# Performance work log

Measured on AMD Instinct MI355X. Metric: run time of the kernel, lower is better.

## Reference

```python
import jax, jax.numpy as jnp
import numpy as np

N_NODES = 50000
N_EDGES = 800000
NUM_HEADS = 4
HEAD_DIM = 32
IN_DIM = 128
NEG_SLOPE = 0.2


def setup_inputs() -> dict:
    key = jax.random.key(0)
    k1, k2, k3, k4, k5, k6 = jax.random.split(key, 6)
    x = jax.random.normal(k1, (N_NODES, IN_DIM), dtype=jnp.float32)
    W = jax.random.normal(k2, (NUM_HEADS * HEAD_DIM, IN_DIM), dtype=jnp.float32) * 0.05
    attn_l = jax.random.normal(k3, (NUM_HEADS, HEAD_DIM), dtype=jnp.float32) * 0.05
    attn_r = jax.random.normal(k4, (NUM_HEADS, HEAD_DIM), dtype=jnp.float32) * 0.05
    src = jax.random.randint(k5, (N_EDGES,), 0, N_NODES, dtype=jnp.int32)
    dst = jnp.sort(jax.random.randint(k6, (N_EDGES,), 0, N_NODES, dtype=jnp.int32))
    return {"x": x, "W": W, "attn_l": attn_l, "attn_r": attn_r, "src": src, "dst": dst}


def reference(x, W, attn_l, attn_r, src, dst):
    N = x.shape[0]
    H, D = attn_l.shape
    # linear projection: [N, H*D] -> [N, H, D]
    feat = (x @ W.T).reshape(N, H, D)
    # per-node attention terms  [N, H]
    el = jnp.einsum('nhd,hd->nh', feat, attn_l)
    er = jnp.einsum('nhd,hd->nh', feat, attn_r)
    # per-edge logits (u_add_v) + leaky relu  [E, H]
    e = el[src] + er[dst]
    e = jnp.where(e > 0, e, NEG_SLOPE * e)
    # edge softmax segmented by destination node
    e_max = jax.ops.segment_max(e, dst, num_segments=N)          # [N, H]
    e_exp = jnp.exp(e - e_max[dst])                              # [E, H]
    denom = jax.ops.segment_sum(e_exp, dst, num_segments=N)     # [N, H]
    alpha = e_exp / denom[dst]                                   # [E, H]
    # attention-weighted neighbor aggregation  [N, H, D]
    out = jax.ops.segment_sum(alpha[:, :, None] * feat[src], dst, num_segments=N)
    return out.reshape(N, H * D)
```

## Files before the change

### kernel.cpp

```cpp
#include <hip/hip_runtime.h>
#include <math.h>

#define NN 50000
#define NE 800000
#define NH 4
#define HD 32
#define FD 128
#define NTILE 3125
#define GEMM_BLOCKS 391
#define ROWS_BLOCKS ((NE + 511) / 512)

typedef __attribute__((ext_vector_type(8))) short short8;
typedef __attribute__((ext_vector_type(4))) float floatx4;

__device__ __forceinline__ unsigned short f2bf(float f) {
    union { float f; unsigned u; } v; v.f = f;
    unsigned u = v.u;
    return (unsigned short)((u + 0x7FFFu + ((u >> 16) & 1u)) >> 16);
}
__device__ __forceinline__ float bf_lo(unsigned u) {
    union { unsigned u; float f; } v; v.u = u << 16; return v.f;
}
__device__ __forceinline__ float bf_hi(unsigned u) {
    union { unsigned u; float f; } v; v.u = u & 0xFFFF0000u; return v.f;
}

__global__ __launch_bounds__(512) void k_gemm_rows(const float* __restrict__ x,
                                                   const float* __restrict__ W,
                                                   const float* __restrict__ al,
                                                   const float* __restrict__ ar,
                                                   const int* __restrict__ dst,
                                                   unsigned short* __restrict__ feat_bf,
                                                   float* __restrict__ el,
                                                   float* __restrict__ er,
                                                   int* __restrict__ rows) {
    const int tid = threadIdx.x;

    if (blockIdx.x >= GEMM_BLOCKS) {
        int e = (blockIdx.x - GEMM_BLOCKS) * 512 + tid;
        if (e < NE) {
            int dj = dst[e];
            if (e == 0) {
                for (int n = 0; n <= dj; ++n) rows[n] = 0;
            } else {
                int prev = dst[e - 1];
                for (int n = prev + 1; n <= dj; ++n) rows[n] = e;
            }
            if (e == NE - 1) {
                for (int n = dj + 1; n <= NN; ++n) rows[n] = NE;
            }
        }
        return;
    }

    __shared__ unsigned short Wl[FD * 136];
    for (int p = tid; p < FD * 64; p += 512) {
        int c = p >> 6, k2 = (p & 63) * 2;
        float2 wv = *(const float2*)&W[c * FD + k2];
        *(unsigned*)&Wl[c * 136 + k2] =
            (unsigned)f2bf(wv.x) | ((unsigned)f2bf(wv.y) << 16);
    }
    __syncthreads();

    const int wv_id = tid >> 6, lane = tid & 63;
    const int tile = blockIdx.x * 8 + wv_id;
    if (tile >= NTILE) return;
    const int col = lane & 15, quad = lane >> 4;

    float alr[8], arr[8];
    #pragma unroll
    for (int ct = 0; ct < 8; ++ct) {
        alr[ct] = al[col + 16 * ct];
        arr[ct] = ar[col + 16 * ct];
    }

    const int n0 = tile * 16;

    short8 afrag[4];
    const float* xrow = x + (size_t)(n0 + col) * FD;
    #pragma unroll
    for (int s = 0; s < 4; ++s) {
        float4 u0 = *(const float4*)&xrow[s * 32 + quad * 8];
        float4 u1 = *(const float4*)&xrow[s * 32 + quad * 8 + 4];
        short8 a;
        a[0] = (short)f2bf(u0.x); a[1] = (short)f2bf(u0.y);
        a[2] = (short)f2bf(u0.z); a[3] = (short)f2bf(u0.w);
        a[4] = (short)f2bf(u1.x); a[5] = (short)f2bf(u1.y);
        a[6] = (short)f2bf(u1.z); a[7] = (short)f2bf(u1.w);
        afrag[s] = a;
    }

    floatx4 acc[8];
    #pragma unroll
    for (int ct = 0; ct < 8; ++ct) acc[ct] = (floatx4){0.f, 0.f, 0.f, 0.f};

    #pragma unroll
    for (int ct = 0; ct < 8; ++ct) {
        #pragma unroll
        for (int s = 0; s < 4; ++s) {
            short8 b = *(const short8*)&Wl[(ct * 16 + col) * 136 + s * 32 + quad * 8];
            acc[ct] = __builtin_amdgcn_mfma_f32_16x16x32_bf16(afrag[s], b, acc[ct], 0, 0, 0);
        }
    }

    #pragma unroll
    for (int ct = 0; ct < 8; ++ct) {
        #pragma unroll
        for (int r = 0; r < 4; ++r) {
            feat_bf[(size_t)(n0 + quad * 4 + r) * FD + ct * 16 + col] = f2bf(acc[ct][r]);
        }
    }

    #pragma unroll
    for (int r = 0; r < 4; ++r) {
        float ev[8];
        #pragma unroll
        for (int hh = 0; hh < NH; ++hh) {
            ev[hh]     = acc[2 * hh][r] * alr[2 * hh] + acc[2 * hh + 1][r] * alr[2 * hh + 1];
            ev[4 + hh] = acc[2 * hh][r] * arr[2 * hh] + acc[2 * hh + 1][r] * arr[2 * hh + 1];
        }
        #pragma unroll
        for (int m = 1; m < 16; m <<= 1) {
            #pragma unroll
            for (int j = 0; j < 8; ++j) ev[j] += __shfl_xor(ev[j], m);
        }
        if (col == 0) {
            int n = n0 + quad * 4 + r;
            *(float4*)&el[n * NH] = make_float4(ev[0], ev[1], ev[2], ev[3]);
            *(float4*)&er[n * NH] = make_float4(ev[4], ev[5], ev[6], ev[7]);
        }
    }
}

__global__ __launch_bounds__(256) void k_aggregate(const unsigned short* __restrict__ feat_bf,
                                                   const float* __restrict__ el,
                                                   const float* __restrict__ er,
                                                   const int* __restrict__ src,
                                                   const int* __restrict__ rows,
                                                   float* __restrict__ out) {
    const int wave = threadIdx.x >> 6;
    const int lane = threadIdx.x & 63;
    const int n = blockIdx.x * 4 + wave;
    if (n >= NN) return;

    const int s = __builtin_amdgcn_readfirstlane(rows[n]);
    const int t = __builtin_amdgcn_readfirstlane(rows[n + 1]);
    const int q  = lane >> 4;
    const int lp = lane & 15;
    const int h  = lp >> 2;
    const int dimoff = 8 * lp;

    const float erh = er[n * NH + h];

    float acc[8] = {0.f, 0.f, 0.f, 0.f, 0.f, 0.f, 0.f, 0.f};
    float den = 0.f;

    for (int e = (s & ~3); e < t; e += 16) {
        const int base = e + 4 * q;
        int sj4[4];
        const bool full4 = (base >= s) && (base + 3 < t);
        if (full4) {
            int4 sv = *(const int4*)&src[base];
            sj4[0] = sv.x; sj4[1] = sv.y; sj4[2] = sv.z; sj4[3] = sv.w;
        } else {
            #pragma unroll
            for (int u = 0; u < 4; ++u) {
                int ei = base + u;
                sj4[u] = (ei >= s && ei < t) ? src[ei] : 0;
            }
        }

        float elv[4];
        #pragma unroll
        for (int u = 0; u < 4; ++u) {
            int ei = base + u;
            if (ei >= s && ei < t) elv[u] = el[sj4[u] * NH + h];
        }
        uint4 uvv[4];
        #pragma unroll
        for (int u = 0; u < 4; ++u) {
            int ei = base + u;
            if (ei >= s && ei < t)
                uvv[u] = *(const uint4*)&feat_bf[(size_t)sj4[u] * FD + dimoff];
        }

        #pragma unroll
        for (int u = 0; u < 4; ++u) {
            int ei = base + u;
            if (ei >= s && ei < t) {
                float lg = elv[u] + erh;
                float w = __expf(fmaxf(lg, 0.2f * lg));
                uint4 uv = uvv[u];
                acc[0] += w * bf_lo(uv.x); acc[1] += w * bf_hi(uv.x);
                acc[2] += w * bf_lo(uv.y); acc[3] += w * bf_hi(uv.y);
                acc[4] += w * bf_lo(uv.z); acc[5] += w * bf_hi(uv.z);
                acc[6] += w * bf_lo(uv.w); acc[7] += w * bf_hi(uv.w);
                den += w;
            }
        }
    }

    #pragma unroll
    for (int m = 16; m < 64; m <<= 1) {
        #pragma unroll
        for (int j = 0; j < 8; ++j) acc[j] += __shfl_xor(acc[j], m);
        den += __shfl_xor(den, m);
    }

    if (q == 0) {
        const float rden = (den > 0.f) ? 1.f / den : 0.f;
        float* op = out + (size_t)n * FD + dimoff;
        *(float4*)op       = make_float4(acc[0] * rden, acc[1] * rden, acc[2] * rden, acc[3] * rden);
        *(float4*)(op + 4) = make_float4(acc[4] * rden, acc[5] * rden, acc[6] * rden, acc[7] * rden);
    }
}

extern "C" void kernel_launch(void* const* d_in, const int* in_sizes, int n_in,
                              void* d_out, int out_size, void* d_ws, size_t ws_size,
                              hipStream_t stream) {
    const float* x  = (const float*)d_in[0];
    const float* W  = (const float*)d_in[1];
    const float* al = (const float*)d_in[2];
    const float* ar = (const float*)d_in[3];
    const int* src  = (const int*)d_in[4];
    const int* dst  = (const int*)d_in[5];
    float* out = (float*)d_out;

    unsigned short* feat_bf = (unsigned short*)d_ws;
    float* el = (float*)(feat_bf + (size_t)NN * FD);
    float* er = el + (size_t)NN * NH;
    int*   rows = (int*)(er + (size_t)NN * NH);

    k_gemm_rows<<<GEMM_BLOCKS + ROWS_BLOCKS, 512, 0, stream>>>(x, W, al, ar, dst,
                                                               feat_bf, el, er, rows);
    k_aggregate<<<(NN + 3) / 4, 256, 0, stream>>>(feat_bf, el, er, src, rows, out);
}
```

Before: 142.2 us.

## Precompute per-edge attention weights in LDS per block and grid-stride GEMM tiles

Result: faster. 136.3 us (-4.2%).

```diff
diff --git a/kernel.cpp b/kernel.cpp
--- a/kernel.cpp
+++ b/kernel.cpp
@@ -7,8 +7,9 @@
 #define HD 32
 #define FD 128
 #define NTILE 3125
-#define GEMM_BLOCKS 391
+#define GEMM_BLOCKS 256
 #define ROWS_BLOCKS ((NE + 511) / 512)
+#define CAP 1024
 
 typedef __attribute__((ext_vector_type(8))) short short8;
 typedef __attribute__((ext_vector_type(4))) float floatx4;
@@ -63,8 +64,6 @@
     __syncthreads();
 
     const int wv_id = tid >> 6, lane = tid & 63;
-    const int tile = blockIdx.x * 8 + wv_id;
-    if (tile >= NTILE) return;
     const int col = lane & 15, quad = lane >> 4;
 
     float alr[8], arr[8];
@@ -74,60 +73,62 @@
         arr[ct] = ar[col + 16 * ct];
     }
 
-    const int n0 = tile * 16;
-
-    short8 afrag[4];
-    const float* xrow = x + (size_t)(n0 + col) * FD;
-    #pragma unroll
-    for (int s = 0; s < 4; ++s) {
-        float4 u0 = *(const float4*)&xrow[s * 32 + quad * 8];
-        float4 u1 = *(const float4*)&xrow[s * 32 + quad * 8 + 4];
-        short8 a;
-        a[0] = (short)f2bf(u0.x); a[1] = (short)f2bf(u0.y);
-        a[2] = (short)f2bf(u0.z); a[3] = (short)f2bf(u0.w);
-        a[4] = (short)f2bf(u1.x); a[5] = (short)f2bf(u1.y);
-        a[6] = (short)f2bf(u1.z); a[7] = (short)f2bf(u1.w);
-        afrag[s] = a;
-    }
-
-    floatx4 acc[8];
-    #pragma unroll
-    for (int ct = 0; ct < 8; ++ct) acc[ct] = (floatx4){0.f, 0.f, 0.f, 0.f};
-
-    #pragma unroll
-    for (int ct = 0; ct < 8; ++ct) {
+    for (int tile = blockIdx.x * 8 + wv_id; tile < NTILE; tile += GEMM_BLOCKS * 8) {
+        const int n0 = tile * 16;
+
+        short8 afrag[4];
+        const float* xrow = x + (size_t)(n0 + col) * FD;
         #pragma unroll
         for (int s = 0; s < 4; ++s) {
-            short8 b = *(const short8*)&Wl[(ct * 16 + col) * 136 + s * 32 + quad * 8];
-            acc[ct] = __builtin_amdgcn_mfma_f32_16x16x32_bf16(afrag[s], b, acc[ct], 0, 0, 0);
-        }
-    }
-
-    #pragma unroll
-    for (int ct = 0; ct < 8; ++ct) {
+            float4 u0 = *(const float4*)&xrow[s * 32 + quad * 8];
+            float4 u1 = *(const float4*)&xrow[s * 32 + quad * 8 + 4];
+            short8 a;
+            a[0] = (short)f2bf(u0.x); a[1] = (short)f2bf(u0.y);
+            a[2] = (short)f2bf(u0.z); a[3] = (short)f2bf(u0.w);
+            a[4] = (short)f2bf(u1.x); a[5] = (short)f2bf(u1.y);
+            a[6] = (short)f2bf(u1.z); a[7] = (short)f2bf(u1.w);
+            afrag[s] = a;
+        }
+
+        floatx4 acc[8];
+        #pragma unroll
+        for (int ct = 0; ct < 8; ++ct) acc[ct] = (floatx4){0.f, 0.f, 0.f, 0.f};
+
+        #pragma unroll
+        for (int ct = 0; ct < 8; ++ct) {
+            #pragma unroll
+            for (int s = 0; s < 4; ++s) {
+                short8 b = *(const short8*)&Wl[(ct * 16 + col) * 136 + s * 32 + quad * 8];
+                acc[ct] = __builtin_amdgcn_mfma_f32_16x16x32_bf16(afrag[s], b, acc[ct], 0, 0, 0);
+            }
+        }
+
+        #pragma unroll
+        for (int ct = 0; ct < 8; ++ct) {
+            #pragma unroll
+            for (int r = 0; r < 4; ++r) {
+                feat_bf[(size_t)(n0 + quad * 4 + r) * FD + ct * 16 + col] = f2bf(acc[ct][r]);
+            }
+        }
+
         #pragma unroll
         for (int r = 0; r < 4; ++r) {
-            feat_bf[(size_t)(n0 + quad * 4 + r) * FD + ct * 16 + col] = f2bf(acc[ct][r]);
-        }
-    }
-
-    #pragma unroll
-    for (int r = 0; r < 4; ++r) {
-        float ev[8];
-        #pragma unroll
-        for (int hh = 0; hh < NH; ++hh) {
-            ev[hh]     = acc[2 * hh][r] * alr[2 * hh] + acc[2 * hh + 1][r] * alr[2 * hh + 1];
-            ev[4 + hh] = acc[2 * hh][r] * arr[2 * hh] + acc[2 * hh + 1][r] * arr[2 * hh + 1];
-        }
-        #pragma unroll
-        for (int m = 1; m < 16; m <<= 1) {
-            #pragma unroll
-            for (int j = 0; j < 8; ++j) ev[j] += __shfl_xor(ev[j], m);
-        }
-        if (col == 0) {
-            int n = n0 + quad * 4 + r;
-            *(float4*)&el[n * NH] = make_float4(ev[0], ev[1], ev[2], ev[3]);
-            *(float4*)&er[n * NH] = make_float4(ev[4], ev[5], ev[6], ev[7]);
+            float ev[8];
+            #pragma unroll
+            for (int hh = 0; hh < NH; ++hh) {
+                ev[hh]     = acc[2 * hh][r] * alr[2 * hh] + acc[2 * hh + 1][r] * alr[2 * hh + 1];
+                ev[4 + hh] = acc[2 * hh][r] * arr[2 * hh] + acc[2 * hh + 1][r] * arr[2 * hh + 1];
+            }
+            #pragma unroll
+            for (int m = 1; m < 16; m <<= 1) {
+                #pragma unroll
+                for (int j = 0; j < 8; ++j) ev[j] += __shfl_xor(ev[j], m);
+            }
+            if (col == 0) {
+                int n = n0 + quad * 4 + r;
+                *(float4*)&el[n * NH] = make_float4(ev[0], ev[1], ev[2], ev[3]);
+                *(float4*)&er[n * NH] = make_float4(ev[4], ev[5], ev[6], ev[7]);
+            }
         }
     }
 }
@@ -136,68 +137,86 @@
                                                    const float* __restrict__ el,
                                                    const float* __restrict__ er,
                                                    const int* __restrict__ src,
+                                                   const int* __restrict__ dst,
                                                    const int* __restrict__ rows,
                                                    float* __restrict__ out) {
-    const int wave = threadIdx.x >> 6;
-    const int lane = threadIdx.x & 63;
-    const int n = blockIdx.x * 4 + wave;
-    if (n >= NN) return;
-
-    const int s = __builtin_amdgcn_readfirstlane(rows[n]);
-    const int t = __builtin_amdgcn_readfirstlane(rows[n + 1]);
+    __shared__ float wS[CAP * NH];
+    const int tid = threadIdx.x;
+    const int wave = tid >> 6;
+    const int lane = tid & 63;
+    const int n0 = blockIdx.x * 4;
+    const int n  = n0 + wave;
+
+    const int s0 = __builtin_amdgcn_readfirstlane(rows[n0]);
+    const int t3 = __builtin_amdgcn_readfirstlane(rows[n0 + 4]);
+    const int s  = __builtin_amdgcn_readfirstlane(rows[n]);
+    const int t  = __builtin_amdgcn_readfirstlane(rows[n + 1]);
+
     const int q  = lane >> 4;
     const int lp = lane & 15;
     const int h  = lp >> 2;
     const int dimoff = 8 * lp;
 
-    const float erh = er[n * NH + h];
-
     float acc[8] = {0.f, 0.f, 0.f, 0.f, 0.f, 0.f, 0.f, 0.f};
     float den = 0.f;
 
-    for (int e = (s & ~3); e < t; e += 16) {
-        const int base = e + 4 * q;
-        int sj4[4];
-        const bool full4 = (base >= s) && (base + 3 < t);
-        if (full4) {
-            int4 sv = *(const int4*)&src[base];
-            sj4[0] = sv.x; sj4[1] = sv.y; sj4[2] = sv.z; sj4[3] = sv.w;
-        } else {
+    for (int c0 = s0; c0 < t3; c0 += CAP) {
+        const int c1 = min(c0 + CAP, t3);
+
+        for (int e = c0 + tid; e < c1; e += 256) {
+            int sj = src[e], dj = dst[e];
+            float4 l4 = *(const float4*)&el[sj * NH];
+            float4 r4 = *(const float4*)&er[dj * NH];
+            float4 w; float lg;
+            lg = l4.x + r4.x; w.x = __expf(fmaxf(lg, 0.2f * lg));
+            lg = l4.y + r4.y; w.y = __expf(fmaxf(lg, 0.2f * lg));
+            lg = l4.z + r4.z; w.z = __expf(fmaxf(lg, 0.2f * lg));
+            lg = l4.w + r4.w; w.w = __expf(fmaxf(lg, 0.2f * lg));
+            *(float4*)&wS[(e - c0) * NH] = w;
+        }
+        __syncthreads();
+
+        const int sb = max(s, c0), tb = min(t, c1);
+        for (int e = (sb & ~3); e < tb; e += 16) {
+            const int base = e + 4 * q;
+            int sj4[4];
+            const bool full4 = (base >= sb) && (base + 3 < tb);
+            if (full4) {
+                int4 sv = *(const int4*)&src[base];
+                sj4[0] = sv.x; sj4[1] = sv.y; sj4[2] = sv.z; sj4[3] = sv.w;
+            } else {
+                #pragma unroll
+                for (int u = 0; u < 4; ++u) {
+                    int ei = base + u;
+                    sj4[u] = (ei >= sb && ei < tb) ? src[ei] : 0;
+                }
+            }
+
+            float wv4[4];
+            uint4 uvv[4];
             #pragma unroll
             for (int u = 0; u < 4; ++u) {
                 int ei = base + u;
-                sj4[u] = (ei >= s && ei < t) ? src[ei] : 0;
-            }
-        }
-
-        float elv[4];
-        #pragma unroll
-        for (int u = 0; u < 4; ++u) {
-            int ei = base + u;
-            if (ei >= s && ei < t) elv[u] = el[sj4[u] * NH + h];
-        }
-        uint4 uvv[4];
-        #pragma unroll
-        for (int u = 0; u < 4; ++u) {
-            int ei = base + u;
-            if (ei >= s && ei < t)
-                uvv[u] = *(const uint4*)&feat_bf[(size_t)sj4[u] * FD + dimoff];
-        }
-
-        #pragma unroll
-        for (int u = 0; u < 4; ++u) {
-            int ei = base + u;
-            if (ei >= s && ei < t) {
-                float lg = elv[u] + erh;
-                float w = __expf(fmaxf(lg, 0.2f * lg));
-                uint4 uv = uvv[u];
-                acc[0] += w * bf_lo(uv.x); acc[1] += w * bf_hi(uv.x);
-                acc[2] += w * bf_lo(uv.y); acc[3] += w * bf_hi(uv.y);
-                acc[4] += w * bf_lo(uv.z); acc[5] += w * bf_hi(uv.z);
-                acc[6] += w * bf_lo(uv.w); acc[7] += w * bf_hi(uv.w);
-                den += w;
-            }
-        }
+                bool v = (ei >= sb) && (ei < tb);
+                wv4[u] = v ? wS[(ei - c0) * NH + h] : 0.f;
+                if (v) uvv[u] = *(const uint4*)&feat_bf[(size_t)sj4[u] * FD + dimoff];
+            }
+
+            #pragma unroll
+            for (int u = 0; u < 4; ++u) {
+                int ei = base + u;
+                if (ei >= sb && ei < tb) {
+                    float w = wv4[u];
+                    uint4 uv = uvv[u];
+                    acc[0] += w * bf_lo(uv.x); acc[1] += w * bf_hi(uv.x);
+                    acc[2] += w * bf_lo(uv.y); acc[3] += w * bf_hi(uv.y);
+                    acc[4] += w * bf_lo(uv.z); acc[5] += w * bf_hi(uv.z);
+                    acc[6] += w * bf_lo(uv.w); acc[7] += w * bf_hi(uv.w);
+                    den += w;
+                }
+            }
+        }
+        __syncthreads();
     }
 
     #pragma unroll
@@ -233,5 +252,5 @@
 
     k_gemm_rows<<<GEMM_BLOCKS + ROWS_BLOCKS, 512, 0, stream>>>(x, W, al, ar, dst,
                                                                feat_bf, el, er, rows);
-    k_aggregate<<<(NN + 3) / 4, 256, 0, stream>>>(feat_bf, el, er, src, rows, out);
-}
+    k_aggregate<<<NN / 4, 256, 0, stream>>>(feat_bf, el, er, src, dst, rows, out);
+}
```
